# Performance work log

Hardware: AMD Instinct MI355X
Metric: run time of the kernel (lower is better)

Reference implementation:

```python
import jax, jax.numpy as jnp
import numpy as np

# CPC config (mirrors CONFIG in the torch repo)
B, S, D = 16, 128, 256      # batch, seq_len, latent dim
K = 12                      # CONFIG.num_predicts
N = 128                     # CONFIG.negative_samples
W = S - K                   # prediction window


def setup_inputs() -> dict:
    key = jax.random.key(0)
    k1, k2, k3, k4 = jax.random.split(key, 4)
    return {
        "predictions": jax.random.normal(k1, (B, W, K, D), jnp.float32),
        "latent": jax.random.normal(k2, (B, S, D), jnp.float32),
        # negative-sample indices (torch generated these with a torch.Generator)
        "batch_idx": jax.random.randint(k3, (N * W * B,), 0, B, jnp.int32),
        "seq_idx": jax.random.randint(k4, (N * W * B,), 1, S, jnp.int32),
    }


def reference(predictions, latent, batch_idx, seq_idx):
    B_, S_, D_ = latent.shape
    _, W_, K_, _ = predictions.shape
    N_ = batch_idx.shape[0] // (W_ * B_)

    # --- sample_for_prediction: gather negatives -------------------------
    # base_idx: arange(W) broadcast to (B, N, W), flattened (matches torch)
    base = jnp.broadcast_to(jnp.arange(W_, dtype=jnp.int32), (B_, N_, W_)).reshape(-1)
    seq = jnp.remainder(seq_idx + base, S_)
    ext = seq + batch_idx * S_
    neg = latent.reshape(-1, D_)[ext].reshape(B_, N_, W_, D_)  # [B,N,W,D]

    # positives: for step k (1..K), pos_k = latent[:, k : k+W]
    pos_idx = jnp.arange(1, K_ + 1)[:, None] + jnp.arange(W_)[None, :]  # [K,W]
    pos = latent[:, pos_idx]  # [B,K,W,D]

    # --- scores: (pred * sample).mean(dim=-1) as contractions -----------
    inv_d = 1.0 / D_
    pos_s = jnp.einsum('bwkd,bkwd->bkw', predictions, pos) * inv_d        # [B,K,W]
    neg_s = jnp.einsum('bwkd,bnwd->bknw', predictions, neg) * inv_d       # [B,K,N,W]
    logits = jnp.concatenate([pos_s[:, :, None, :], neg_s], axis=2)       # [B,K,1+N,W]

    # --- cross-entropy with target class 0, mean over B*W ---------------
    losses = jnp.mean(jax.nn.logsumexp(logits, axis=2) - logits[:, :, 0, :], axis=(0, 2))  # [K]
    acc = jnp.mean((jnp.argmax(logits, axis=2) == 0).astype(jnp.float32), axis=(0, 2))     # [K]
    return losses, acc
```

## Files before the change

kernel.cpp:

```cpp
#include <hip/hip_runtime.h>

#define BB 16
#define SS 128
#define DD 256
#define KK 12
#define NN 128
#define WW 116

__global__ __launch_bounds__(128, 4)
void cpc_main(const float* __restrict__ pred,
              const float* __restrict__ latent,
              const int* __restrict__ bidx,
              const int* __restrict__ sidx,
              float* __restrict__ out) {
    const int wg = blockIdx.x;
    const int b  = wg / WW;
    const int w  = wg - b * WW;
    const int n  = threadIdx.x;

    const int i   = (b * NN + n) * WW + w;
    const int seq = (sidx[i] + w) & (SS - 1);
    const int ext = seq + bidx[i] * SS;
    const float* __restrict__ lrow = latent + (size_t)ext * DD;
    const float* __restrict__ prow = pred + (size_t)wg * KK * DD;

    float acc[KK];
#pragma unroll
    for (int k = 0; k < KK; ++k) acc[k] = 0.f;

#pragma unroll 4
    for (int d = 0; d < DD; d += 4) {
        const float4 lv = *reinterpret_cast<const float4*>(lrow + d);
#pragma unroll
        for (int k = 0; k < KK; ++k) {
            const float4 pv = *reinterpret_cast<const float4*>(prow + k * DD + d);
            acc[k] = fmaf(pv.x, lv.x, acc[k]);
            acc[k] = fmaf(pv.y, lv.y, acc[k]);
            acc[k] = fmaf(pv.z, lv.z, acc[k]);
            acc[k] = fmaf(pv.w, lv.w, acc[k]);
        }
    }

    constexpr float inv_d = 1.0f / DD;
    __shared__ float sc[KK][NN + 1];
    __shared__ float posv[KK];
#pragma unroll
    for (int k = 0; k < KK; ++k) sc[k][n] = acc[k] * inv_d;

    const int t = threadIdx.x;
    if (t < 96) {
        const int k = t >> 3, g = t & 7;
        const float* pr = pred + ((size_t)wg * KK + k) * DD + g * 32;
        const float* lr = latent + ((size_t)b * SS + (w + k + 1)) * DD + g * 32;
        float s = 0.f;
#pragma unroll
        for (int d = 0; d < 32; d += 4) {
            const float4 pv = *reinterpret_cast<const float4*>(pr + d);
            const float4 lv = *reinterpret_cast<const float4*>(lr + d);
            s = fmaf(pv.x, lv.x, s); s = fmaf(pv.y, lv.y, s);
            s = fmaf(pv.z, lv.z, s); s = fmaf(pv.w, lv.w, s);
        }
        s += __shfl_xor(s, 1);
        s += __shfl_xor(s, 2);
        s += __shfl_xor(s, 4);
        if (g == 0) posv[k] = s * inv_d;
    }
    __syncthreads();

    if (t < 96) {
        const int k = t >> 3, g = t & 7;
        const float p = posv[k];
        float v[16];
        float m = p;
#pragma unroll
        for (int j = 0; j < 16; ++j) {
            v[j] = sc[k][j * 8 + g];
            m = fmaxf(m, v[j]);
        }
        m = fmaxf(m, __shfl_xor(m, 1));
        m = fmaxf(m, __shfl_xor(m, 2));
        m = fmaxf(m, __shfl_xor(m, 4));
        float sum = (g == 0) ? __expf(p - m) : 0.f;
#pragma unroll
        for (int j = 0; j < 16; ++j) sum += __expf(v[j] - m);
        sum += __shfl_xor(sum, 1);
        sum += __shfl_xor(sum, 2);
        sum += __shfl_xor(sum, 4);
        if (g == 0) {
            constexpr float inv_bw = 1.0f / (BB * WW);
            const float lse = m + __logf(sum);
            atomicAdd(&out[k], (lse - p) * inv_bw);
            atomicAdd(&out[KK + k], (p >= m) ? inv_bw : 0.f);
        }
    }
}

extern "C" void kernel_launch(void* const* d_in, const int* in_sizes, int n_in,
                              void* d_out, int out_size, void* d_ws, size_t ws_size,
                              hipStream_t stream) {
    const float* pred   = (const float*)d_in[0];
    const float* latent = (const float*)d_in[1];
    const int*   bidx   = (const int*)d_in[2];
    const int*   sidx   = (const int*)d_in[3];
    float* out = (float*)d_out;
    hipMemsetAsync(out, 0, 2 * KK * sizeof(float), stream);
    cpc_main<<<BB * WW, 128, 0, stream>>>(pred, latent, bidx, sidx, out);
}
```

Baseline: 192.4 us.

## Split D across two thread halves and stage predictions in LDS

Doubles the block to 256 threads, with each half computing partial dot products over half of D. The two partials are combined through shared memory. The block's 12x256 prediction tile is loaded cooperatively into LDS once, replacing repeated global reads from every thread. This doubles the number of active waves for latency hiding, at the cost of extra barriers and about 12KB more LDS per block, which may limit occupancy.

```diff
diff --git a/kernel.cpp b/kernel.cpp
--- a/kernel.cpp
+++ b/kernel.cpp
@@ -7,7 +7,7 @@
 #define NN 128
 #define WW 116
 
-__global__ __launch_bounds__(128, 4)
+__global__ __launch_bounds__(256, 6)
 void cpc_main(const float* __restrict__ pred,
               const float* __restrict__ latent,
               const int* __restrict__ bidx,
@@ -16,20 +16,35 @@
     const int wg = blockIdx.x;
     const int b  = wg / WW;
     const int w  = wg - b * WW;
-    const int n  = threadIdx.x;
+    const int t  = threadIdx.x;
+    const int n  = t & (NN - 1);
+    const int h  = t >> 7;
+
+    __shared__ float predl[KK * DD];
+    __shared__ float sc[KK][NN + 1];
+    __shared__ float posv[KK];
+
+    {
+        const float4* __restrict__ psrc =
+            reinterpret_cast<const float4*>(pred + (size_t)wg * KK * DD);
+        float4* pdst = reinterpret_cast<float4*>(predl);
+#pragma unroll
+        for (int i = 0; i < 3; ++i) pdst[t + i * 256] = psrc[t + i * 256];
+    }
+    __syncthreads();
 
     const int i   = (b * NN + n) * WW + w;
     const int seq = (sidx[i] + w) & (SS - 1);
     const int ext = seq + bidx[i] * SS;
-    const float* __restrict__ lrow = latent + (size_t)ext * DD;
-    const float* __restrict__ prow = pred + (size_t)wg * KK * DD;
+    const float* __restrict__ lrow = latent + (size_t)ext * DD + h * (DD / 2);
+    const float* __restrict__ prow = predl + h * (DD / 2);
 
     float acc[KK];
 #pragma unroll
     for (int k = 0; k < KK; ++k) acc[k] = 0.f;
 
 #pragma unroll 4
-    for (int d = 0; d < DD; d += 4) {
+    for (int d = 0; d < DD / 2; d += 4) {
         const float4 lv = *reinterpret_cast<const float4*>(lrow + d);
 #pragma unroll
         for (int k = 0; k < KK; ++k) {
@@ -42,15 +57,20 @@
     }
 
     constexpr float inv_d = 1.0f / DD;
-    __shared__ float sc[KK][NN + 1];
-    __shared__ float posv[KK];
+    if (h == 1) {
 #pragma unroll
-    for (int k = 0; k < KK; ++k) sc[k][n] = acc[k] * inv_d;
+        for (int k = 0; k < KK; ++k) sc[k][n] = acc[k];
+    }
+    __syncthreads();
+    if (h == 0) {
+#pragma unroll
+        for (int k = 0; k < KK; ++k) sc[k][n] = (acc[k] + sc[k][n]) * inv_d;
+    }
 
-    const int t = threadIdx.x;
-    if (t < 96) {
-        const int k = t >> 3, g = t & 7;
-        const float* pr = pred + ((size_t)wg * KK + k) * DD + g * 32;
+    if (t >= 128 && t < 224) {
+        const int tt = t - 128;
+        const int k = tt >> 3, g = tt & 7;
+        const float* pr = predl + k * DD + g * 32;
         const float* lr = latent + ((size_t)b * SS + (w + k + 1)) * DD + g * 32;
         float s = 0.f;
 #pragma unroll
@@ -104,5 +124,5 @@
     const int*   sidx   = (const int*)d_in[3];
     float* out = (float*)d_out;
     hipMemsetAsync(out, 0, 2 * KK * sizeof(float), stream);
-    cpc_main<<<BB * WW, 128, 0, stream>>>(pred, latent, bidx, sidx, out);
+    cpc_main<<<BB * WW, 256, 0, stream>>>(pred, latent, bidx, sidx, out);
 }
```

Measured after the change: 170.9 us. 11.2% less time.

## Compute negative scores with bf16 split-precision MFMA instead of scalar FMAs

Applied to the files above, without the earlier changes.

Stores predictions as hi/lo bf16 pairs in swizzled shared memory and computes the negative-sample dot products with 16x16x32 bf16 MFMA using a three-term split to approximate fp32 accuracy. The block grows to 256 threads, four waves of 32 negatives each. This targets the scalar FMA bottleneck of the per-thread dot products, at the cost of extra conversion ALU work, more shared memory, and slightly reduced precision, which could flip argmax ties.

```diff
diff --git a/kernel.cpp b/kernel.cpp
--- a/kernel.cpp
+++ b/kernel.cpp
@@ -1,4 +1,5 @@
 #include <hip/hip_runtime.h>
+#include <hip/hip_bf16.h>
 
 #define BB 16
 #define SS 128
@@ -7,7 +8,27 @@
 #define NN 128
 #define WW 116
 
-__global__ __launch_bounds__(128, 4)
+typedef __attribute__((ext_vector_type(8))) short short8;
+typedef __attribute__((ext_vector_type(4))) float f32x4;
+
+__device__ __forceinline__ int swz(int byte_off, int row) {
+    return byte_off ^ ((row & 7) << 4);
+}
+
+__device__ __forceinline__ void cvt_hilo8(const float4 p, const float4 q,
+                                          short8& h, short8& l) {
+    float x[8] = {p.x, p.y, p.z, p.w, q.x, q.y, q.z, q.w};
+#pragma unroll
+    for (int i = 0; i < 8; ++i) {
+        __hip_bfloat16 hb = __float2bfloat16(x[i]);
+        float hf = __bfloat162float(hb);
+        __hip_bfloat16 lb = __float2bfloat16(x[i] - hf);
+        h[i] = __builtin_bit_cast(short, hb);
+        l[i] = __builtin_bit_cast(short, lb);
+    }
+}
+
+__global__ __launch_bounds__(256, 4)
 void cpc_main(const float* __restrict__ pred,
               const float* __restrict__ latent,
               const int* __restrict__ bidx,
@@ -16,47 +37,98 @@
     const int wg = blockIdx.x;
     const int b  = wg / WW;
     const int w  = wg - b * WW;
-    const int n  = threadIdx.x;
+    const int t  = threadIdx.x;
 
-    const int i   = (b * NN + n) * WW + w;
-    const int seq = (sidx[i] + w) & (SS - 1);
-    const int ext = seq + bidx[i] * SS;
-    const float* __restrict__ lrow = latent + (size_t)ext * DD;
-    const float* __restrict__ prow = pred + (size_t)wg * KK * DD;
+    __shared__ short Ahi[16 * DD];
+    __shared__ short Alo[16 * DD];
+    __shared__ float sc[KK][NN + 1];
+    __shared__ float posv[KK];
 
-    float acc[KK];
+    const float* __restrict__ pbase = pred + (size_t)wg * KK * DD;
+
+    if (t < 96) {
+        const int r = t >> 3, seg = t & 7;
+        const float* src = pbase + r * DD + seg * 32;
 #pragma unroll
-    for (int k = 0; k < KK; ++k) acc[k] = 0.f;
-
-#pragma unroll 4
-    for (int d = 0; d < DD; d += 4) {
-        const float4 lv = *reinterpret_cast<const float4*>(lrow + d);
+        for (int c = 0; c < 4; ++c) {
+            float4 p = *reinterpret_cast<const float4*>(src + c * 8);
+            float4 q = *reinterpret_cast<const float4*>(src + c * 8 + 4);
+            short8 h, l;
+            cvt_hilo8(p, q, h, l);
+            const int byte = r * 512 + seg * 64 + c * 16;
+            *reinterpret_cast<short8*>((char*)Ahi + swz(byte, r)) = h;
+            *reinterpret_cast<short8*>((char*)Alo + swz(byte, r)) = l;
+        }
+    } else if (t < 128) {
+        const int u = t - 96;
+        const int r = 12 + (u >> 3), seg = u & 7;
+        const short8 z = {0, 0, 0, 0, 0, 0, 0, 0};
 #pragma unroll
-        for (int k = 0; k < KK; ++k) {
-            const float4 pv = *reinterpret_cast<const float4*>(prow + k * DD + d);
-            acc[k] = fmaf(pv.x, lv.x, acc[k]);
-            acc[k] = fmaf(pv.y, lv.y, acc[k]);
-            acc[k] = fmaf(pv.z, lv.z, acc[k]);
-            acc[k] = fmaf(pv.w, lv.w, acc[k]);
+        for (int c = 0; c < 4; ++c) {
+            const int byte = r * 512 + seg * 64 + c * 16;
+            *reinterpret_cast<short8*>((char*)Ahi + swz(byte, r)) = z;
+            *reinterpret_cast<short8*>((char*)Alo + swz(byte, r)) = z;
         }
     }
 
+    const int wv   = t >> 6;
+    const int lane = t & 63;
+    const int lr   = lane & 15;
+    const int lg   = lane >> 4;
+    const int n0 = wv * 32 + lr;
+    const int n1 = n0 + 16;
+    const int i0 = (b * NN + n0) * WW + w;
+    const int i1 = (b * NN + n1) * WW + w;
+    const int ext0 = ((sidx[i0] + w) & (SS - 1)) + bidx[i0] * SS;
+    const int ext1 = ((sidx[i1] + w) & (SS - 1)) + bidx[i1] * SS;
+    const float* __restrict__ L0 = latent + (size_t)ext0 * DD + lg * 8;
+    const float* __restrict__ L1 = latent + (size_t)ext1 * DD + lg * 8;
+
+    __syncthreads();
+
+    f32x4 acc0 = {0.f, 0.f, 0.f, 0.f};
+    f32x4 acc1 = {0.f, 0.f, 0.f, 0.f};
+    const int abyte = lr * 512 + lg * 16;
+#pragma unroll 2
+    for (int ks = 0; ks < 8; ++ks) {
+        const short8 ah = *reinterpret_cast<const short8*>(
+            (const char*)Ahi + swz(abyte + ks * 64, lr));
+        const short8 al = *reinterpret_cast<const short8*>(
+            (const char*)Alo + swz(abyte + ks * 64, lr));
+        const float4 p0 = *reinterpret_cast<const float4*>(L0 + ks * 32);
+        const float4 q0 = *reinterpret_cast<const float4*>(L0 + ks * 32 + 4);
+        const float4 p1 = *reinterpret_cast<const float4*>(L1 + ks * 32);
+        const float4 q1 = *reinterpret_cast<const float4*>(L1 + ks * 32 + 4);
+        short8 bh0, bl0, bh1, bl1;
+        cvt_hilo8(p0, q0, bh0, bl0);
+        cvt_hilo8(p1, q1, bh1, bl1);
+        acc0 = __builtin_amdgcn_mfma_f32_16x16x32_bf16(ah, bh0, acc0, 0, 0, 0);
+        acc1 = __builtin_amdgcn_mfma_f32_16x16x32_bf16(ah, bh1, acc1, 0, 0, 0);
+        acc0 = __builtin_amdgcn_mfma_f32_16x16x32_bf16(ah, bl0, acc0, 0, 0, 0);
+        acc1 = __builtin_amdgcn_mfma_f32_16x16x32_bf16(ah, bl1, acc1, 0, 0, 0);
+        acc0 = __builtin_amdgcn_mfma_f32_16x16x32_bf16(al, bh0, acc0, 0, 0, 0);
+        acc1 = __builtin_amdgcn_mfma_f32_16x16x32_bf16(al, bh1, acc1, 0, 0, 0);
+    }
+
     constexpr float inv_d = 1.0f / DD;
-    __shared__ float sc[KK][NN + 1];
-    __shared__ float posv[KK];
+    const int krow = lg * 4;
+    if (krow < KK) {
 #pragma unroll
-    for (int k = 0; k < KK; ++k) sc[k][n] = acc[k] * inv_d;
+        for (int r = 0; r < 4; ++r) {
+            sc[krow + r][n0] = acc0[r] * inv_d;
+            sc[krow + r][n1] = acc1[r] * inv_d;
+        }
+    }
 
-    const int t = threadIdx.x;
     if (t < 96) {
         const int k = t >> 3, g = t & 7;
-        const float* pr = pred + ((size_t)wg * KK + k) * DD + g * 32;
-        const float* lr = latent + ((size_t)b * SS + (w + k + 1)) * DD + g * 32;
+        const float* pr = pbase + k * DD + g * 32;
+        const float* lrow = latent + ((size_t)b * SS + (w + k + 1)) * DD + g * 32;
         float s = 0.f;
 #pragma unroll
         for (int d = 0; d < 32; d += 4) {
             const float4 pv = *reinterpret_cast<const float4*>(pr + d);
-            const float4 lv = *reinterpret_cast<const float4*>(lr + d);
+            const float4 lv = *reinterpret_cast<const float4*>(lrow + d);
             s = fmaf(pv.x, lv.x, s); s = fmaf(pv.y, lv.y, s);
             s = fmaf(pv.z, lv.z, s); s = fmaf(pv.w, lv.w, s);
         }
@@ -104,5 +176,5 @@
     const int*   sidx   = (const int*)d_in[3];
     float* out = (float*)d_out;
     hipMemsetAsync(out, 0, 2 * KK * sizeof(float), stream);
-    cpc_main<<<BB * WW, 128, 0, stream>>>(pred, latent, bidx, sidx, out);
+    cpc_main<<<BB * WW, 256, 0, stream>>>(pred, latent, bidx, sidx, out);
 }
```

Measured after the change: 160.7 us. 16.5% less time.
